# Kernel optimization log

Hardware: AMD Instinct MI355X
Metric: run time of the kernel (lower is better)

Reference implementation:

```python
import jax, jax.numpy as jnp
import numpy as np

N, IN_DIM, OUT_DIM = 4096, 512, 512
H, D = 8, OUT_DIM // 8          # num_heads, head_dim
ALPHA = 0.2                     # leaky relu slope
NEG = -9e15
EPS = 1e-5


def setup_inputs() -> dict:
    key = jax.random.key(0)
    k1, k2, k3, k4 = jax.random.split(key, 4)
    x = jax.random.normal(k1, (N, IN_DIM), dtype=jnp.float32)
    adj = jax.random.randint(k2, (N, N), 0, 2, dtype=jnp.int32)
    # scale params like nn.Linear default init (~1/sqrt(fan_in)) to keep scores sane
    W = jax.random.normal(k3, (OUT_DIM, IN_DIM), dtype=jnp.float32) / np.sqrt(IN_DIM)
    a = jax.random.normal(k4, (2 * D,), dtype=jnp.float32) / np.sqrt(2 * D)
    gamma = jnp.ones((OUT_DIM,), dtype=jnp.float32)
    beta = jnp.zeros((OUT_DIM,), dtype=jnp.float32)
    return {"x": x, "adj": adj, "W": W, "a": a, "gamma": gamma, "beta": beta}


def reference(x, adj, W, a, gamma, beta):
    n = x.shape[0]
    Wh = (x @ W.T).reshape(n, H, D)                       # [N, H, D]
    a_src, a_dst = a[:D], a[D:]                           # shared across heads
    s_src = jnp.einsum('jhd,d->jh', Wh, a_src)            # [N, H] source term
    s_dst = jnp.einsum('ihd,d->ih', Wh, a_dst)            # [N, H] dest term
    # e[i, j, h] = leakyrelu(a_src . Wh[j,h] + a_dst . Wh[i,h]); row i = dst, col j = src
    e = jax.nn.leaky_relu(s_dst[:, None, :] + s_src[None, :, :], negative_slope=ALPHA)
    e = jnp.where((adj > 0)[:, :, None], e, NEG)          # mask non-edges
    attn = jax.nn.softmax(e, axis=1)                      # softmax over source nodes j
    h_prime = jnp.einsum('ijh,jhd->ihd', attn, Wh).reshape(n, H * D)  # [N, out_dim]
    # BatchNorm1d (training-mode batch statistics, biased variance)
    mean = jnp.mean(h_prime, axis=0)
    var = jnp.var(h_prime, axis=0)
    h_prime = gamma * (h_prime - mean) * jax.lax.rsqrt(var + EPS) + beta
    return jax.nn.relu(h_prime)
```

## Files before the change

### kernel.cpp

```cpp
#include <hip/hip_runtime.h>
#include <hip/hip_bf16.h>
#include <hip/hip_fp16.h>
#include <stdint.h>


typedef __attribute__((ext_vector_type(4))) float f32x4;
typedef __attribute__((ext_vector_type(8))) short s16x8;
typedef __attribute__((ext_vector_type(2))) _Float16 h2v;

#define LOG2E 1.4426950408889634f

static __device__ __forceinline__ ushort f2bf(float f) {
  union { float f; uint32_t u; } v; v.f = f;
  uint32_t r = (v.u + 0x7FFFu + ((v.u >> 16) & 1u)) >> 16;
  return (ushort)r;
}

static __device__ __forceinline__ short bf16b(float f) {
  __hip_bfloat16 h = __float2bfloat16(f);
  union { __hip_bfloat16 h; short s; } c; c.h = h;
  return c.s;
}

static __device__ __forceinline__ float bf2f(ushort u) {
  union { uint32_t u; float f; } c; c.u = ((uint32_t)u) << 16;
  return c.f;
}

static __device__ __forceinline__ ushort hbits(float f) {
  union { _Float16 h; ushort u; } c; c.h = (_Float16)f;
  return c.u;
}

static __device__ __forceinline__ h2v u2h2(uint32_t u) {
  union { uint32_t u; h2v h; } c; c.u = u; return c.h;
}
static __device__ __forceinline__ uint32_t h22u(h2v h) {
  union { uint32_t u; h2v h; } c; c.h = h; return c.u;
}

static __device__ __forceinline__ uint32_t mask2f16(uint32_t w, int q) {
#if __has_builtin(__builtin_amdgcn_sbfe) && __has_builtin(__builtin_amdgcn_perm)
  const uint32_t mlo = (uint32_t)__builtin_amdgcn_sbfe((int)w, q, 1);
  const uint32_t mhi = (uint32_t)__builtin_amdgcn_sbfe((int)w, q + 1, 1);
  return __builtin_amdgcn_perm(mhi, mlo, 0x07060100u);
#else
  return (((w >> q) & 1u) | (((w >> q) & 2u) << 15)) * 0xFFFFu;
#endif
}

static __device__ __forceinline__ void gl_lds16(const ushort* g, ushort* l) {
  __builtin_amdgcn_global_load_lds(
      (const __attribute__((address_space(1))) unsigned int*)(g),
      (__attribute__((address_space(3))) unsigned int*)(l), 16, 0, 0);
}

__global__ __launch_bounds__(256) void k_prep(const float* __restrict__ x,
                                              const float* __restrict__ W,
                                              const int* __restrict__ adj,
                                              ushort* __restrict__ xb,
                                              ushort* __restrict__ wb,
                                              unsigned long long* __restrict__ maskw,
                                              float* __restrict__ stats) {
  const int t = threadIdx.x;
  if (blockIdx.x < 2304) {
    const int idx = (blockIdx.x * 256 + t) * 4;
    const int NX = 4096 * 512;
    if (idx < NX) {
      float4 v = *(const float4*)(x + idx);
      ushort4 o; o.x = f2bf(v.x); o.y = f2bf(v.y); o.z = f2bf(v.z); o.w = f2bf(v.w);
      *(ushort4*)(xb + idx) = o;
    } else {
      const int k = idx - NX;
      float4 v = *(const float4*)(W + k);
      ushort4 o; o.x = f2bf(v.x); o.y = f2bf(v.y); o.z = f2bf(v.z); o.w = f2bf(v.w);
      *(ushort4*)(wb + k) = o;
    }
  } else {
    const int pb = blockIdx.x - 2304;
    if (pb == 0) {
      stats[t] = 0.f; stats[t + 256] = 0.f; stats[t + 512] = 0.f; stats[t + 768] = 0.f;
    }
    const size_t base = (size_t)pb * 8192;
    const int lane = t & 63;
#pragma unroll 4
    for (int it = 0; it < 32; ++it) {
      const size_t elem = base + it * 256 + t;
      unsigned long long b = __ballot(adj[elem] > 0);
      if (lane == 0) maskw[elem >> 6] = b;
    }
  }
}

__global__ __launch_bounds__(256) void k_gemm(const ushort* __restrict__ xb,
                                              const ushort* __restrict__ wb,
                                              const float* __restrict__ a,
                                              ushort* __restrict__ WhT,
                                              ushort* __restrict__ EsT,
                                              ushort* __restrict__ es2T,
                                              float* __restrict__ rT) {
  __shared__ ushort bt[64 * 512];
  float* tl = (float*)bt;
  const int lane = threadIdx.x & 63;
  const int wv = threadIdx.x >> 6;
  const int l15 = lane & 15, lg = lane >> 4;
  const int m0 = blockIdx.x * 64;
  const int h = blockIdx.y;
  const int n0 = h * 64;

#pragma unroll
  for (int it = 0; it < 16; ++it) {
    const int col = it * 4 + wv;
    const ushort* src = wb + (size_t)(n0 + col) * 512 + (lane ^ (col & 7)) * 8;
    gl_lds16(src, &bt[col * 512]);
  }
  __syncthreads();

  const ushort* ap = xb + (size_t)(m0 + wv * 16 + l15) * 512 + lg * 8;
  f32x4 acc[4] = {};
  for (int k0 = 0; k0 < 512; k0 += 32) {
    s16x8 av = *(const s16x8*)(ap + k0);
#pragma unroll
    for (int ct = 0; ct < 4; ++ct) {
      const int col = ct * 16 + l15;
      s16x8 b = *(const s16x8*)((const char*)bt + col * 1024 +
                                (((k0 + lg * 8) * 2) ^ ((col & 7) << 4)));
      acc[ct] = __builtin_amdgcn_mfma_f32_16x16x32_bf16(av, b, acc[ct], 0, 0, 0);
    }
  }
  float aS[4], aD[4];
#pragma unroll
  for (int ct = 0; ct < 4; ++ct) {
    aS[ct] = a[ct * 16 + l15];
    aD[ct] = a[64 + ct * 16 + l15];
  }
#pragma unroll
  for (int r = 0; r < 4; ++r) {
    float s1 = acc[0][r] * aS[0] + acc[1][r] * aS[1] + acc[2][r] * aS[2] + acc[3][r] * aS[3];
    float s2 = acc[0][r] * aD[0] + acc[1][r] * aD[1] + acc[2][r] * aD[2] + acc[3][r] * aD[3];
#pragma unroll
    for (int off = 1; off < 16; off <<= 1) {
      s1 += __shfl_xor(s1, off);
      s2 += __shfl_xor(s2, off);
    }
    if (l15 == 0) {
      const int row = m0 + wv * 16 + lg * 4 + r;
      const float aa = s1 * LOG2E;
      const float bb = s2 * LOG2E;
      EsT[h * 4096 + row]  = hbits(__builtin_amdgcn_exp2f(aa));
      es2T[h * 4096 + row] = hbits(__builtin_amdgcn_exp2f(0.2f * aa));
      rT[h * 4096 + row]   = __builtin_amdgcn_exp2f(-0.8f * bb);
    }
  }
  __syncthreads();
#pragma unroll
  for (int ct = 0; ct < 4; ++ct)
#pragma unroll
    for (int r = 0; r < 4; ++r)
      tl[(ct * 16 + l15) * 65 + wv * 16 + lg * 4 + r] = acc[ct][r];
  __syncthreads();
  const int c = threadIdx.x >> 2, mb = (threadIdx.x & 3) * 16;
  s16x8 o0, o1;
#pragma unroll
  for (int k = 0; k < 8; ++k) o0[k] = (short)hbits(tl[c * 65 + mb + k]);
#pragma unroll
  for (int k = 0; k < 8; ++k) o1[k] = (short)hbits(tl[c * 65 + mb + 8 + k]);
  *(s16x8*)(WhT + (size_t)(n0 + c) * 4096 + m0 + mb) = o0;
  *(s16x8*)(WhT + (size_t)(n0 + c) * 4096 + m0 + mb + 8) = o1;
}

__global__ __launch_bounds__(512, 4) void k_attn(
    const uint32_t* __restrict__ mask32,
    const ushort* __restrict__ WhT,
    const ushort* __restrict__ EsT,
    const ushort* __restrict__ es2T,
    const float* __restrict__ rT,
    ushort* __restrict__ num,
    float* __restrict__ lbuf) {
  __shared__ ushort tile[4][4096];
  __shared__ uint32_t mask_s[256 * 33];
  __shared__ uint32_t Es_s[512];
  __shared__ uint32_t es2_s[512];

  const int t = threadIdx.x;
  const int lane = t & 63, wv = t >> 6;
  const int l15 = lane & 15, lg = lane >> 4;
  const int h = blockIdx.y;
  const int jh = blockIdx.x & 3;
  const int ih = blockIdx.x >> 2;
  const int i0b = ih * 256;
  const int j0 = jh * 1024;

  if (t < 128) {
    ((uint4*)Es_s)[t] = ((const uint4*)EsT)[(h * 4096 + j0) / 8 + t];
  } else if (t < 256) {
    ((uint4*)es2_s)[t - 128] = ((const uint4*)es2T)[(h * 4096 + j0) / 8 + t - 128];
  }
  {
    const int r = t >> 1, part = t & 1;
    const uint32_t* src = mask32 + (size_t)(i0b + r) * 128 + jh * 32 + part * 16;
    uint32_t* dst = &mask_s[r * 33 + part * 16];
#pragma unroll
    for (int k = 0; k < 4; ++k)
      *(int4*)(dst + k * 4) = *(const int4*)(src + k * 4);
  }
  const int cg = (wv << 3) + (lane >> 3);
  const int gg = (lane & 7) ^ (cg & 7);
  const ushort* sbase = WhT + (size_t)(h * 64 + cg) * 4096 + j0 + gg * 8;

  gl_lds16(sbase, &tile[0][wv * 512]);
  gl_lds16(sbase + 64, &tile[1][wv * 512]);
  gl_lds16(sbase + 128, &tile[2][wv * 512]);
  __syncthreads();

  const int rloc = wv * 32 + l15;
  const float r0f = rT[h * 4096 + i0b + rloc];
  const float r1f = rT[h * 4096 + i0b + rloc + 16];
  const h2v r02 = {(_Float16)r0f, (_Float16)r0f};
  const h2v r12 = {(_Float16)r1f, (_Float16)r1f};

  f32x4 acc[2][4] = {};
  f32x4 accd0 = {}, accd1 = {};
  s16x8 bones;
  {
    const short v = (l15 == 0) ? (short)0x3C00 : (short)0;
    bones[0] = v; bones[1] = v; bones[2] = v; bones[3] = v;
    bones[4] = v; bones[5] = v; bones[6] = v; bones[7] = v;
  }

#pragma unroll 1
  for (int c = 0; c < 16; ++c) {
    if (c < 14)       asm volatile("s_waitcnt vmcnt(2)" ::: "memory");
    else if (c == 14) asm volatile("s_waitcnt vmcnt(1)" ::: "memory");
    else              asm volatile("s_waitcnt vmcnt(0)" ::: "memory");
    __builtin_amdgcn_s_barrier();
    if (c < 13) gl_lds16(sbase + (size_t)(c + 3) * 64, &tile[(c + 3) & 3][wv * 512]);
    const char* tb = (const char*)&tile[c & 3][0];
#pragma unroll
    for (int half = 0; half < 2; ++half) {
      const int jsub = half * 32;
      const uint4 e4 = *(const uint4*)&Es_s[c * 32 + (jsub >> 1) + lg * 4];
      const uint4 f4 = *(const uint4*)&es2_s[c * 32 + (jsub >> 1) + lg * 4];
      const uint32_t w0 = mask_s[rloc * 33 + c * 2 + half] >> (lg * 8);
      const uint32_t w1 = mask_s[(rloc + 16) * 33 + c * 2 + half] >> (lg * 8);
      s16x8 b[4];
#pragma unroll
      for (int ct = 0; ct < 4; ++ct) {
        const int col = ct * 16 + l15;
        b[ct] = *(const s16x8*)(tb + col * 128 + ((jsub * 2 + lg * 16) ^ ((col & 7) << 4)));
      }
      union { s16x8 v8; uint32_t u32[4]; } pa0, pa1;
#pragma unroll
      for (int q2 = 0; q2 < 4; ++q2) {
        const int q = q2 * 2;
        const h2v e2 = u2h2(((const uint32_t*)&e4)[q2]);
        const h2v f2 = u2h2(((const uint32_t*)&f4)[q2]);
        const h2v t0 = __builtin_elementwise_max(e2, r02 * f2);
        const h2v t1 = __builtin_elementwise_max(e2, r12 * f2);
        pa0.u32[q2] = mask2f16(w0, q) & h22u(t0);
        pa1.u32[q2] = mask2f16(w1, q) & h22u(t1);
      }
      accd0 = __builtin_amdgcn_mfma_f32_16x16x32_f16(pa0.v8, bones, accd0, 0, 0, 0);
      accd1 = __builtin_amdgcn_mfma_f32_16x16x32_f16(pa1.v8, bones, accd1, 0, 0, 0);
#pragma unroll
      for (int ct = 0; ct < 4; ++ct) {
        acc[0][ct] = __builtin_amdgcn_mfma_f32_16x16x32_f16(pa0.v8, b[ct], acc[0][ct], 0, 0, 0);
        acc[1][ct] = __builtin_amdgcn_mfma_f32_16x16x32_f16(pa1.v8, b[ct], acc[1][ct], 0, 0, 0);
      }
    }
  }

  if (l15 == 0) {
    float* lb = &lbuf[((size_t)jh * 8 + h) * 4096 + i0b + rloc];
#pragma unroll
    for (int r = 0; r < 4; ++r) lb[lg * 4 + r] = accd0[r];
#pragma unroll
    for (int r = 0; r < 4; ++r) lb[16 + lg * 4 + r] = accd1[r];
  }
  ushort* np = num + (size_t)jh * 4096 * 512;
#pragma unroll
  for (int rs = 0; rs < 2; ++rs)
#pragma unroll
    for (int ct = 0; ct < 4; ++ct)
#pragma unroll
      for (int r = 0; r < 4; ++r)
        np[(size_t)(i0b + wv * 32 + rs * 16 + lg * 4 + r) * 512 + h * 64 + ct * 16 + l15] =
            (ushort)bf16b(acc[rs][ct][r]);
}

__global__ __launch_bounds__(512) void k_stats(const ushort* __restrict__ num,
                                               const float* __restrict__ lbuf,
                                               ushort* __restrict__ hpb,
                                               float* __restrict__ stats) {
  __shared__ float linv_s[128];
  const int t = threadIdx.x;
  const int r0 = blockIdx.x * 16;
  if (t < 128) {
    const int r = r0 + (t >> 3), hh = t & 7;
    float l = 0.f;
#pragma unroll
    for (int s = 0; s < 4; ++s) l += lbuf[((size_t)s * 8 + hh) * 4096 + r];
    linv_s[t] = 1.0f / l;
  }
  __syncthreads();
  const int c = t;
  const int hh = c >> 6;
  float s1 = 0.f, s2 = 0.f;
  for (int rr = 0; rr < 16; ++rr) {
    const int r = r0 + rr;
    float nsum = 0.f;
#pragma unroll
    for (int s = 0; s < 4; ++s)
      nsum += bf2f(num[(size_t)s * 4096 * 512 + (size_t)r * 512 + c]);
    const float v = nsum * linv_s[rr * 8 + hh];
    hpb[(size_t)r * 512 + c] = (ushort)bf16b(v);
    s1 += v; s2 += v * v;
  }
  atomicAdd(&stats[c], s1);
  atomicAdd(&stats[512 + c], s2);
}

__global__ __launch_bounds__(256) void k_apply(const ushort* __restrict__ hpb,
                                               const float* __restrict__ stats,
                                               const float* __restrict__ gamma,
                                               const float* __restrict__ beta,
                                               float* __restrict__ out) {
  const size_t idx8 = ((size_t)blockIdx.x * 256 + threadIdx.x) * 8;
  const int c0 = (int)(idx8 & 511);
  s16x8 hv = *(const s16x8*)(hpb + idx8);
#pragma unroll
  for (int k = 0; k < 8; ++k) {
    const int cc = c0 + k;
    const float mean = stats[cc] * (1.f / 4096.f);
    const float var = stats[512 + cc] * (1.f / 4096.f) - mean * mean;
    const float v = bf2f((ushort)hv[k]);
    const float val = (v - mean) * rsqrtf(var + 1e-5f) * gamma[cc] + beta[cc];
    out[idx8 + k] = fmaxf(val, 0.f);
  }
}

extern "C" void kernel_launch(void* const* d_in, const int* in_sizes, int n_in,
                              void* d_out, int out_size, void* d_ws, size_t ws_size,
                              hipStream_t stream) {
  const float* x = (const float*)d_in[0];
  const int* adj = (const int*)d_in[1];
  const float* W = (const float*)d_in[2];
  const float* a = (const float*)d_in[3];
  const float* gamma = (const float*)d_in[4];
  const float* beta = (const float*)d_in[5];
  float* out = (float*)d_out;

  char* ws = (char*)d_ws;
  size_t off = 0;
  auto alloc = [&](size_t bytes) -> void* {
    void* p = ws + off;
    off += (bytes + 255) & ~(size_t)255;
    return p;
  };
  ushort* WhT   = (ushort*)alloc((size_t)512 * 4096 * 2);
  ushort* EsT   = (ushort*)alloc((size_t)8 * 4096 * 2);
  ushort* es2T  = (ushort*)alloc((size_t)8 * 4096 * 2);
  float*  rT    = (float*)alloc((size_t)8 * 4096 * 4);
  unsigned long long* maskw = (unsigned long long*)alloc((size_t)4096 * 64 * 8);
  float*  lbuf  = (float*)alloc((size_t)32 * 4096 * 4);
  ushort* hpb   = (ushort*)alloc((size_t)4096 * 512 * 2);
  float*  stats = (float*)alloc((size_t)1024 * 4);
  const size_t ov = off;
  ushort* xb = (ushort*)(ws + ov);
  ushort* wb = (ushort*)(ws + ov + (size_t)4096 * 512 * 2);
  ushort* num = (ushort*)(ws + ov);

  hipLaunchKernelGGL(k_prep, dim3(4352), dim3(256), 0, stream,
                     x, W, adj, xb, wb, maskw, stats);
  hipLaunchKernelGGL(k_gemm, dim3(64, 8), dim3(256), 0, stream, xb, wb, a,
                     WhT, EsT, es2T, rT);
  hipLaunchKernelGGL(k_attn, dim3(64, 8), dim3(512), 0, stream,
                     (const uint32_t*)maskw, WhT, EsT, es2T, rT, num, lbuf);
  hipLaunchKernelGGL(k_stats, dim3(256), dim3(512), 0, stream, num, lbuf, hpb, stats);
  hipLaunchKernelGGL(k_apply, dim3(1024), dim3(256), 0, stream, hpb, stats, gamma, beta, out);
}
```

Measured before the change: 73.71 us.

## Halve attention block to 4 waves, each computing 64 rows for more B-fragment reuse

The attention kernel now runs 256 threads (4 waves) per block instead of 512. Each wave handles 64 destination rows instead of 32, so every B fragment read from LDS feeds 16 MFMAs instead of 8. Global-to-LDS loads are split into two issues per thread, and the wait counts are adjusted to match. This cuts LDS read traffic and the repeated exp-term math per MFMA, at the cost of doubling the accumulator registers (64 floats for acc) and possibly lowering occupancy and latency hiding.

After: 75.39 us. 1.02x slower.

```diff
diff --git a/kernel.cpp b/kernel.cpp
--- a/kernel.cpp
+++ b/kernel.cpp
@@ -169,7 +169,7 @@
   *(s16x8*)(WhT + (size_t)(n0 + c) * 4096 + m0 + mb + 8) = o1;
 }
 
-__global__ __launch_bounds__(512, 4) void k_attn(
+__global__ __launch_bounds__(256, 2) void k_attn(
     const uint32_t* __restrict__ mask32,
     const ushort* __restrict__ WhT,
     const ushort* __restrict__ EsT,
@@ -193,34 +193,41 @@
 
   if (t < 128) {
     ((uint4*)Es_s)[t] = ((const uint4*)EsT)[(h * 4096 + j0) / 8 + t];
-  } else if (t < 256) {
+  } else {
     ((uint4*)es2_s)[t - 128] = ((const uint4*)es2T)[(h * 4096 + j0) / 8 + t - 128];
   }
   {
-    const int r = t >> 1, part = t & 1;
-    const uint32_t* src = mask32 + (size_t)(i0b + r) * 128 + jh * 32 + part * 16;
-    uint32_t* dst = &mask_s[r * 33 + part * 16];
-#pragma unroll
-    for (int k = 0; k < 4; ++k)
+    const uint32_t* src = mask32 + (size_t)(i0b + t) * 128 + jh * 32;
+    uint32_t* dst = &mask_s[t * 33];
+#pragma unroll
+    for (int k = 0; k < 8; ++k)
       *(int4*)(dst + k * 4) = *(const int4*)(src + k * 4);
   }
-  const int cg = (wv << 3) + (lane >> 3);
-  const int gg = (lane & 7) ^ (cg & 7);
-  const ushort* sbase = WhT + (size_t)(h * 64 + cg) * 4096 + j0 + gg * 8;
-
-  gl_lds16(sbase, &tile[0][wv * 512]);
-  gl_lds16(sbase + 64, &tile[1][wv * 512]);
-  gl_lds16(sbase + 128, &tile[2][wv * 512]);
-  __syncthreads();
-
-  const int rloc = wv * 32 + l15;
-  const float r0f = rT[h * 4096 + i0b + rloc];
-  const float r1f = rT[h * 4096 + i0b + rloc + 16];
-  const h2v r02 = {(_Float16)r0f, (_Float16)r0f};
-  const h2v r12 = {(_Float16)r1f, (_Float16)r1f};
-
-  f32x4 acc[2][4] = {};
-  f32x4 accd0 = {}, accd1 = {};
+  const int cg0 = (wv << 4) + (lane >> 3);
+  const int cg1 = cg0 + 8;
+  const ushort* sb0 = WhT + (size_t)(h * 64 + cg0) * 4096 + j0 +
+                      (((lane & 7) ^ (cg0 & 7)) * 8);
+  const ushort* sb1 = WhT + (size_t)(h * 64 + cg1) * 4096 + j0 +
+                      (((lane & 7) ^ (cg1 & 7)) * 8);
+
+#pragma unroll
+  for (int c = 0; c < 3; ++c) {
+    gl_lds16(sb0 + c * 64, &tile[c][(wv * 16) * 64]);
+    gl_lds16(sb1 + c * 64, &tile[c][(wv * 16 + 8) * 64]);
+  }
+  __syncthreads();
+
+  const int rloc = wv * 64 + l15;
+  float rf[4];
+  h2v r2[4];
+#pragma unroll
+  for (int k = 0; k < 4; ++k) {
+    rf[k] = rT[h * 4096 + i0b + rloc + k * 16];
+    r2[k] = (h2v){(_Float16)rf[k], (_Float16)rf[k]};
+  }
+
+  f32x4 acc[4][4] = {};
+  f32x4 accd[4] = {};
   s16x8 bones;
   {
     const short v = (l15 == 0) ? (short)0x3C00 : (short)0;
@@ -230,62 +237,69 @@
 
 #pragma unroll 1
   for (int c = 0; c < 16; ++c) {
-    if (c < 14)       asm volatile("s_waitcnt vmcnt(2)" ::: "memory");
-    else if (c == 14) asm volatile("s_waitcnt vmcnt(1)" ::: "memory");
+    if (c <= 13)      asm volatile("s_waitcnt vmcnt(4)" ::: "memory");
+    else if (c == 14) asm volatile("s_waitcnt vmcnt(2)" ::: "memory");
     else              asm volatile("s_waitcnt vmcnt(0)" ::: "memory");
     __builtin_amdgcn_s_barrier();
-    if (c < 13) gl_lds16(sbase + (size_t)(c + 3) * 64, &tile[(c + 3) & 3][wv * 512]);
+    if (c < 13) {
+      gl_lds16(sb0 + (size_t)(c + 3) * 64, &tile[(c + 3) & 3][(wv * 16) * 64]);
+      gl_lds16(sb1 + (size_t)(c + 3) * 64, &tile[(c + 3) & 3][(wv * 16 + 8) * 64]);
+    }
     const char* tb = (const char*)&tile[c & 3][0];
 #pragma unroll
     for (int half = 0; half < 2; ++half) {
       const int jsub = half * 32;
       const uint4 e4 = *(const uint4*)&Es_s[c * 32 + (jsub >> 1) + lg * 4];
       const uint4 f4 = *(const uint4*)&es2_s[c * 32 + (jsub >> 1) + lg * 4];
-      const uint32_t w0 = mask_s[rloc * 33 + c * 2 + half] >> (lg * 8);
-      const uint32_t w1 = mask_s[(rloc + 16) * 33 + c * 2 + half] >> (lg * 8);
+      uint32_t w[4];
+#pragma unroll
+      for (int k = 0; k < 4; ++k)
+        w[k] = mask_s[(rloc + k * 16) * 33 + c * 2 + half] >> (lg * 8);
       s16x8 b[4];
 #pragma unroll
       for (int ct = 0; ct < 4; ++ct) {
         const int col = ct * 16 + l15;
         b[ct] = *(const s16x8*)(tb + col * 128 + ((jsub * 2 + lg * 16) ^ ((col & 7) << 4)));
       }
-      union { s16x8 v8; uint32_t u32[4]; } pa0, pa1;
+      union { s16x8 v8; uint32_t u32[4]; } pa[4];
 #pragma unroll
       for (int q2 = 0; q2 < 4; ++q2) {
         const int q = q2 * 2;
         const h2v e2 = u2h2(((const uint32_t*)&e4)[q2]);
         const h2v f2 = u2h2(((const uint32_t*)&f4)[q2]);
-        const h2v t0 = __builtin_elementwise_max(e2, r02 * f2);
-        const h2v t1 = __builtin_elementwise_max(e2, r12 * f2);
-        pa0.u32[q2] = mask2f16(w0, q) & h22u(t0);
-        pa1.u32[q2] = mask2f16(w1, q) & h22u(t1);
+#pragma unroll
+        for (int k = 0; k < 4; ++k) {
+          const h2v tk = __builtin_elementwise_max(e2, r2[k] * f2);
+          pa[k].u32[q2] = mask2f16(w[k], q) & h22u(tk);
+        }
       }
-      accd0 = __builtin_amdgcn_mfma_f32_16x16x32_f16(pa0.v8, bones, accd0, 0, 0, 0);
-      accd1 = __builtin_amdgcn_mfma_f32_16x16x32_f16(pa1.v8, bones, accd1, 0, 0, 0);
-#pragma unroll
-      for (int ct = 0; ct < 4; ++ct) {
-        acc[0][ct] = __builtin_amdgcn_mfma_f32_16x16x32_f16(pa0.v8, b[ct], acc[0][ct], 0, 0, 0);
-        acc[1][ct] = __builtin_amdgcn_mfma_f32_16x16x32_f16(pa1.v8, b[ct], acc[1][ct], 0, 0, 0);
-      }
+#pragma unroll
+      for (int k = 0; k < 4; ++k)
+        accd[k] = __builtin_amdgcn_mfma_f32_16x16x32_f16(pa[k].v8, bones, accd[k], 0, 0, 0);
+#pragma unroll
+      for (int ct = 0; ct < 4; ++ct)
+#pragma unroll
+        for (int k = 0; k < 4; ++k)
+          acc[k][ct] = __builtin_amdgcn_mfma_f32_16x16x32_f16(pa[k].v8, b[ct], acc[k][ct], 0, 0, 0);
     }
   }
 
   if (l15 == 0) {
     float* lb = &lbuf[((size_t)jh * 8 + h) * 4096 + i0b + rloc];
 #pragma unroll
-    for (int r = 0; r < 4; ++r) lb[lg * 4 + r] = accd0[r];
-#pragma unroll
-    for (int r = 0; r < 4; ++r) lb[16 + lg * 4 + r] = accd1[r];
+    for (int k = 0; k < 4; ++k)
+#pragma unroll
+      for (int r = 0; r < 4; ++r) lb[k * 16 + lg * 4 + r] = accd[k][r];
   }
   ushort* np = num + (size_t)jh * 4096 * 512;
 #pragma unroll
-  for (int rs = 0; rs < 2; ++rs)
+  for (int k = 0; k < 4; ++k)
 #pragma unroll
     for (int ct = 0; ct < 4; ++ct)
 #pragma unroll
       for (int r = 0; r < 4; ++r)
-        np[(size_t)(i0b + wv * 32 + rs * 16 + lg * 4 + r) * 512 + h * 64 + ct * 16 + l15] =
-            (ushort)bf16b(acc[rs][ct][r]);
+        np[(size_t)(i0b + rloc - l15 + k * 16 + lg * 4 + r) * 512 + h * 64 + ct * 16 + l15] =
+            (ushort)bf16b(acc[k][ct][r]);
 }
 
 __global__ __launch_bounds__(512) void k_stats(const ushort* __restrict__ num,
@@ -374,7 +388,7 @@
                      x, W, adj, xb, wb, maskw, stats);
   hipLaunchKernelGGL(k_gemm, dim3(64, 8), dim3(256), 0, stream, xb, wb, a,
                      WhT, EsT, es2T, rT);
-  hipLaunchKernelGGL(k_attn, dim3(64, 8), dim3(512), 0, stream,
+  hipLaunchKernelGGL(k_attn, dim3(64, 8), dim3(256), 0, stream,
                      (const uint32_t*)maskw, WhT, EsT, es2T, rT, num, lbuf);
   hipLaunchKernelGGL(k_stats, dim3(256), dim3(512), 0, stream, num, lbuf, hpb, stats);
   hipLaunchKernelGGL(k_apply, dim3(1024), dim3(256), 0, stream, hpb, stats, gamma, beta, out);
```
